# Kernel optimization log

Measured on AMD Instinct MI355X. Metric: run time of the kernel, lower is better.

Reference implementation:

```python
import jax, jax.numpy as jnp
import numpy as np

DIM = 128
BATCH = 1024


def _init_linear(key, fan_in, fan_out):
    kw, kb = jax.random.split(key)
    bound = 1.0 / np.sqrt(fan_in)
    W = jax.random.uniform(kw, (fan_in, fan_out), jnp.float32, -bound, bound)
    b = jax.random.uniform(kb, (fan_out,), jnp.float32, -bound, bound)
    return W, b


def setup_inputs() -> dict:
    key = jax.random.key(0)
    kx, ky, k1, k2, k3, k4 = jax.random.split(key, 6)
    x = jax.random.normal(kx, (BATCH, DIM), jnp.float32)
    y = jax.random.normal(ky, (BATCH, DIM), jnp.float32)
    W1, b1 = _init_linear(k1, 2 * DIM, 128)
    W2, b2 = _init_linear(k2, 128, 64)
    W3, b3 = _init_linear(k3, 64, 8)
    W4, b4 = _init_linear(k4, 8, 1)
    return {"x": x, "y": y, "W1": W1, "b1": b1, "W2": W2, "b2": b2,
            "W3": W3, "b3": b3, "W4": W4, "b4": b4}


def reference(x, y, W1, b1, W2, b2, W3, b3, W4, b4):
    # Original: pairs[i, j] = concat(x[j], y[i]); scores -> [B, B]; return transpose,
    # i.e. out[a, b] = f(concat(x[a], y[b])).
    # Split first linear algebraically: concat(x, y) @ W1 = x @ W1[:d] + y @ W1[d:].
    d = x.shape[1]
    xa = x @ W1[:d]          # [B, 128]
    yb = y @ W1[d:]          # [B, 128]
    h = jax.nn.relu(xa[:, None, :] + yb[None, :, :] + b1)  # [B, B, 128]
    h = jax.nn.relu(h @ W2 + b2)                            # [B, B, 64]
    h = jax.nn.relu(h @ W3 + b3)                            # [B, B, 8]
    out = (h @ W4 + b4)[..., 0]                             # [B, B]
    return out
```

## Files before the change

### kernel.cpp

```cpp
#include <hip/hip_runtime.h>
#include <hip/hip_bf16.h>

typedef float f32x4 __attribute__((ext_vector_type(4)));
typedef float f32x16 __attribute__((ext_vector_type(16)));
typedef short s16x8 __attribute__((ext_vector_type(8)));
typedef unsigned int u32x4 __attribute__((ext_vector_type(4)));

__device__ __forceinline__ short f2bf(float v) {
    __hip_bfloat16 h = __float2bfloat16(v);
    return __builtin_bit_cast(short, h);
}
__device__ __forceinline__ unsigned cvtpk(float lo, float hi) {
    unsigned r;
    asm("v_cvt_pk_bf16_f32 %0, %1, %2" : "=v"(r) : "v"(lo), "v"(hi));
    return r;
}
__device__ __forceinline__ void swap32(unsigned &x, unsigned &y) {
    asm("v_permlane32_swap_b32 %0, %1" : "+v"(x), "+v"(y));
}

__global__ __launch_bounds__(128) void precompute_kernel(
    const float* __restrict__ x, const float* __restrict__ y,
    const float* __restrict__ W1, const float* __restrict__ b1,
    float* __restrict__ xa, float* __restrict__ yb)
{
    __shared__ float rows[8][128];
    const int bid = blockIdx.x;
    const int k = threadIdx.x;
    const bool is_x = bid < 128;
    const int r0 = (is_x ? bid : bid - 128) * 8;
    const float* src = (is_x ? x : y) + (size_t)r0 * 128;
    const float* w = is_x ? W1 : (W1 + 128 * 128);
#pragma unroll
    for (int r = 0; r < 8; ++r) rows[r][k] = src[r * 128 + k];
    __syncthreads();
    float acc[8];
    const float bias = is_x ? b1[k] : 0.0f;
#pragma unroll
    for (int r = 0; r < 8; ++r) acc[r] = bias;
    for (int d = 0; d < 128; ++d) {
        float wv = w[d * 128 + k];
#pragma unroll
        for (int r = 0; r < 8; ++r) acc[r] = fmaf(rows[r][d], wv, acc[r]);
    }
    float* dst = (is_x ? xa : yb) + (size_t)r0 * 128 + k;
#pragma unroll
    for (int r = 0; r < 8; ++r) dst[r * 128] = acc[r];
}

__global__ __launch_bounds__(256, 2) void fused_kernel(
    const float* __restrict__ xa, const float* __restrict__ yb,
    const float* __restrict__ W2, const float* __restrict__ b2,
    const float* __restrict__ W3, const float* __restrict__ b3,
    const float* __restrict__ W4, const float* __restrict__ b4,
    float* __restrict__ out)
{
    __shared__ float xa_lds[16 * 128];
    __shared__ __align__(16) short w3_lds[4 * 64 * 8];

    const int tid = threadIdx.x;
    const int bid = blockIdx.x;
    const int a_chunk = bid >> 3;
    const int bq = bid & 7;
    const int wave = tid >> 6;
    const int lane = tid & 63;
    const int half = lane >> 5;
    const int m = lane & 31;
    const int bg = bq * 4 + wave;

    {
        const f32x4* xsrc = (const f32x4*)(xa + (size_t)a_chunk * 16 * 128);
        f32x4* dst = (f32x4*)xa_lds;
        dst[tid] = xsrc[tid];
        dst[tid + 256] = xsrc[tid + 256];
    }
    {
        int l = tid & 63, s = tid >> 6;
        int row = l & 31;
        int krow = s * 16 + (l >> 5) * 8;
        u32x4 q;
#pragma unroll
        for (int jj = 0; jj < 4; ++jj) {
            float lo = (row < 8) ? W3[(krow + 2 * jj) * 8 + row] : 0.f;
            float hi = (row < 8) ? W3[(krow + 2 * jj + 1) * 8 + row] : 0.f;
            q[jj] = cvtpk(lo, hi);
        }
        *(u32x4*)&w3_lds[tid * 8] = q;
    }

    f32x4 yv0[8], yv1[8];
    {
        const float* yrow = yb + (size_t)(bg * 32 + m) * 128 + half * 8;
#pragma unroll
        for (int s = 0; s < 8; ++s) {
            yv0[s] = *(const f32x4*)&yrow[s * 16];
            yv1[s] = *(const f32x4*)&yrow[s * 16 + 4];
        }
    }

    s16x8 W2a[2][8];
#pragma unroll
    for (int mt = 0; mt < 2; ++mt)
#pragma unroll
        for (int s = 0; s < 8; ++s)
#pragma unroll
            for (int j = 0; j < 8; ++j)
                W2a[mt][s][j] = f2bf(W2[(s * 16 + half * 8 + j) * 64 + mt * 32 + m]);

    f32x16 b2v0, b2v1;
#pragma unroll
    for (int r = 0; r < 16; ++r) {
        int f = (r & 3) + 8 * (r >> 2) + 4 * half;
        b2v0[r] = b2[f];
        b2v1[r] = b2[f + 32];
    }
    const f32x16 fz = {};
    float b3v[4], w4v[4];
#pragma unroll
    for (int j = 0; j < 4; ++j) {
        b3v[j] = b3[j + 4 * half];
        w4v[j] = W4[j + 4 * half];
    }
    const float b4s = b4[0];

    __syncthreads();

    const short* w3p = &w3_lds[lane * 8];
    float* outp = out + (size_t)(a_chunk * 16) * 1024 + bg * 32 + m;

    for (int ai = 0; ai < 16; ++ai) {
        const float* xr = &xa_lds[ai * 128 + half * 8];

        s16x8 bfr[8];
#pragma unroll
        for (int s = 0; s < 8; ++s) {
            f32x4 x0 = *(const f32x4*)&xr[s * 16];
            f32x4 x1 = *(const f32x4*)&xr[s * 16 + 4];
            f32x4 h0 = x0 + yv0[s];
            f32x4 h1 = x1 + yv1[s];
            u32x4 q;
            q.x = cvtpk(fmaxf(h0.x, 0.f), fmaxf(h0.y, 0.f));
            q.y = cvtpk(fmaxf(h0.z, 0.f), fmaxf(h0.w, 0.f));
            q.z = cvtpk(fmaxf(h1.x, 0.f), fmaxf(h1.y, 0.f));
            q.w = cvtpk(fmaxf(h1.z, 0.f), fmaxf(h1.w, 0.f));
            bfr[s] = __builtin_bit_cast(s16x8, q);
        }
        __builtin_amdgcn_sched_barrier(0);

        __builtin_amdgcn_s_setprio(1);
        f32x16 c20 = __builtin_amdgcn_mfma_f32_32x32x16_bf16(W2a[0][0], bfr[0], b2v0, 0, 0, 0);
        f32x16 c21 = __builtin_amdgcn_mfma_f32_32x32x16_bf16(W2a[1][0], bfr[0], b2v1, 0, 0, 0);
#pragma unroll
        for (int s = 1; s < 8; ++s) {
            c20 = __builtin_amdgcn_mfma_f32_32x32x16_bf16(W2a[0][s], bfr[s], c20, 0, 0, 0);
            c21 = __builtin_amdgcn_mfma_f32_32x32x16_bf16(W2a[1][s], bfr[s], c21, 0, 0, 0);
        }
        __builtin_amdgcn_s_setprio(0);

        unsigned P[8], Q[8];
#pragma unroll
        for (int i = 0; i < 8; ++i) {
            P[i] = cvtpk(fmaxf(c20[2 * i], 0.f), fmaxf(c20[2 * i + 1], 0.f));
            Q[i] = cvtpk(fmaxf(c21[2 * i], 0.f), fmaxf(c21[2 * i + 1], 0.f));
        }
        s16x8 bf3[4];
        {
            unsigned w0 = P[0], w2 = P[2]; swap32(w0, w2);
            unsigned w1 = P[1], w3 = P[3]; swap32(w1, w3);
            u32x4 t; t.x = w0; t.y = w1; t.z = w2; t.w = w3;
            bf3[0] = __builtin_bit_cast(s16x8, t);
            unsigned v0 = P[4], v2 = P[6]; swap32(v0, v2);
            unsigned v1 = P[5], v3 = P[7]; swap32(v1, v3);
            u32x4 u; u.x = v0; u.y = v1; u.z = v2; u.w = v3;
            bf3[1] = __builtin_bit_cast(s16x8, u);
            unsigned a0 = Q[0], a2 = Q[2]; swap32(a0, a2);
            unsigned a1 = Q[1], a3 = Q[3]; swap32(a1, a3);
            u32x4 t2; t2.x = a0; t2.y = a1; t2.z = a2; t2.w = a3;
            bf3[2] = __builtin_bit_cast(s16x8, t2);
            unsigned e0 = Q[4], e2 = Q[6]; swap32(e0, e2);
            unsigned e1 = Q[5], e3 = Q[7]; swap32(e1, e3);
            u32x4 u2; u2.x = e0; u2.y = e1; u2.z = e2; u2.w = e3;
            bf3[3] = __builtin_bit_cast(s16x8, u2);
        }

        __builtin_amdgcn_s_setprio(1);
        f32x16 c3 = __builtin_amdgcn_mfma_f32_32x32x16_bf16(
            *(const s16x8*)(w3p + 0 * 512), bf3[0], fz, 0, 0, 0);
#pragma unroll
        for (int s = 1; s < 4; ++s)
            c3 = __builtin_amdgcn_mfma_f32_32x32x16_bf16(
                *(const s16x8*)(w3p + s * 512), bf3[s], c3, 0, 0, 0);
        __builtin_amdgcn_s_setprio(0);

        float p = 0.f;
#pragma unroll
        for (int j = 0; j < 4; ++j)
            p = fmaf(fmaxf(c3[j] + b3v[j], 0.f), w4v[j], p);
        unsigned pu = __builtin_bit_cast(unsigned, p);
        unsigned pv = pu;
        asm("" : "+v"(pv));
        swap32(pu, pv);
        float r = __builtin_bit_cast(float, pu) + __builtin_bit_cast(float, pv) + b4s;
        if (half == 0)
            outp[(size_t)ai * 1024] = r;
    }
}

extern "C" void kernel_launch(void* const* d_in, const int* in_sizes, int n_in,
                              void* d_out, int out_size, void* d_ws, size_t ws_size,
                              hipStream_t stream) {
    const float* x  = (const float*)d_in[0];
    const float* y  = (const float*)d_in[1];
    const float* W1 = (const float*)d_in[2];
    const float* b1 = (const float*)d_in[3];
    const float* W2 = (const float*)d_in[4];
    const float* b2 = (const float*)d_in[5];
    const float* W3 = (const float*)d_in[6];
    const float* b3 = (const float*)d_in[7];
    const float* W4 = (const float*)d_in[8];
    const float* b4 = (const float*)d_in[9];
    float* out = (float*)d_out;

    float* xa = (float*)d_ws;
    float* yb = xa + 1024 * 128;

    precompute_kernel<<<dim3(256), dim3(128), 0, stream>>>(x, y, W1, b1, xa, yb);
    fused_kernel<<<dim3(512), dim3(256), 0, stream>>>(xa, yb, W2, b2, W3, b3, W4, b4, out);
}
```

Before: 44.17 us.

## Interleave two independent rows per iteration and stage biases in LDS

The fused loop now processes two x rows (ai and ai+8) per iteration, interleaving their MFMA chains so the two independent accumulator streams can hide MFMA dependency latency. The b2/b3 bias vectors move from per-thread registers into LDS and are reloaded each iteration to cut register pressure. The W3 fragments are hoisted, and the setprio and sched_barrier hints are dropped. The cost is more live registers for the doubled bfr and accumulators, which may threaten the occupancy of 2 waves implied by the launch bounds.

```diff
diff --git a/kernel.cpp b/kernel.cpp
--- a/kernel.cpp
+++ b/kernel.cpp
@@ -57,6 +57,8 @@
 {
     __shared__ float xa_lds[16 * 128];
     __shared__ __align__(16) short w3_lds[4 * 64 * 8];
+    __shared__ __align__(64) float b2_lds[64];
+    __shared__ __align__(64) float b3_lds[32];
 
     const int tid = threadIdx.x;
     const int bid = blockIdx.x;
@@ -87,6 +89,10 @@
         }
         *(u32x4*)&w3_lds[tid * 8] = q;
     }
+    if (tid < 64)
+        b2_lds[tid] = b2[(tid & 3) + 8 * ((tid >> 2) & 3) + 4 * ((tid >> 4) & 1) + 32 * (tid >> 5)];
+    if (tid < 32)
+        b3_lds[tid] = ((tid & 15) < 4) ? b3[(tid & 3) + 4 * (tid >> 4)] : 0.f;
 
     f32x4 yv0[8], yv1[8];
     {
@@ -107,20 +113,9 @@
             for (int j = 0; j < 8; ++j)
                 W2a[mt][s][j] = f2bf(W2[(s * 16 + half * 8 + j) * 64 + mt * 32 + m]);
 
-    f32x16 b2v0, b2v1;
-#pragma unroll
-    for (int r = 0; r < 16; ++r) {
-        int f = (r & 3) + 8 * (r >> 2) + 4 * half;
-        b2v0[r] = b2[f];
-        b2v1[r] = b2[f + 32];
-    }
-    const f32x16 fz = {};
-    float b3v[4], w4v[4];
-#pragma unroll
-    for (int j = 0; j < 4; ++j) {
-        b3v[j] = b3[j + 4 * half];
-        w4v[j] = W4[j + 4 * half];
-    }
+    float w4v[4];
+#pragma unroll
+    for (int j = 0; j < 4; ++j) w4v[j] = W4[j + 4 * half];
     const float b4s = b4[0];
 
     __syncthreads();
@@ -128,81 +123,128 @@
     const short* w3p = &w3_lds[lane * 8];
     float* outp = out + (size_t)(a_chunk * 16) * 1024 + bg * 32 + m;
 
-    for (int ai = 0; ai < 16; ++ai) {
-        const float* xr = &xa_lds[ai * 128 + half * 8];
-
-        s16x8 bfr[8];
-#pragma unroll
-        for (int s = 0; s < 8; ++s) {
-            f32x4 x0 = *(const f32x4*)&xr[s * 16];
-            f32x4 x1 = *(const f32x4*)&xr[s * 16 + 4];
-            f32x4 h0 = x0 + yv0[s];
-            f32x4 h1 = x1 + yv1[s];
-            u32x4 q;
-            q.x = cvtpk(fmaxf(h0.x, 0.f), fmaxf(h0.y, 0.f));
-            q.y = cvtpk(fmaxf(h0.z, 0.f), fmaxf(h0.w, 0.f));
-            q.z = cvtpk(fmaxf(h1.x, 0.f), fmaxf(h1.y, 0.f));
-            q.w = cvtpk(fmaxf(h1.z, 0.f), fmaxf(h1.w, 0.f));
-            bfr[s] = __builtin_bit_cast(s16x8, q);
-        }
-        __builtin_amdgcn_sched_barrier(0);
-
-        __builtin_amdgcn_s_setprio(1);
-        f32x16 c20 = __builtin_amdgcn_mfma_f32_32x32x16_bf16(W2a[0][0], bfr[0], b2v0, 0, 0, 0);
-        f32x16 c21 = __builtin_amdgcn_mfma_f32_32x32x16_bf16(W2a[1][0], bfr[0], b2v1, 0, 0, 0);
+    for (int ai = 0; ai < 8; ++ai) {
+        s16x8 bfrA[8], bfrB[8];
+        {
+            const float* xrA = &xa_lds[ai * 128 + half * 8];
+            const float* xrB = &xa_lds[(ai + 8) * 128 + half * 8];
+#pragma unroll
+            for (int s = 0; s < 8; ++s) {
+                f32x4 a0 = *(const f32x4*)&xrA[s * 16] + yv0[s];
+                f32x4 a1 = *(const f32x4*)&xrA[s * 16 + 4] + yv1[s];
+                u32x4 qa;
+                qa.x = cvtpk(fmaxf(a0.x, 0.f), fmaxf(a0.y, 0.f));
+                qa.y = cvtpk(fmaxf(a0.z, 0.f), fmaxf(a0.w, 0.f));
+                qa.z = cvtpk(fmaxf(a1.x, 0.f), fmaxf(a1.y, 0.f));
+                qa.w = cvtpk(fmaxf(a1.z, 0.f), fmaxf(a1.w, 0.f));
+                bfrA[s] = __builtin_bit_cast(s16x8, qa);
+                f32x4 b0 = *(const f32x4*)&xrB[s * 16] + yv0[s];
+                f32x4 b1 = *(const f32x4*)&xrB[s * 16 + 4] + yv1[s];
+                u32x4 qb;
+                qb.x = cvtpk(fmaxf(b0.x, 0.f), fmaxf(b0.y, 0.f));
+                qb.y = cvtpk(fmaxf(b0.z, 0.f), fmaxf(b0.w, 0.f));
+                qb.z = cvtpk(fmaxf(b1.x, 0.f), fmaxf(b1.y, 0.f));
+                qb.w = cvtpk(fmaxf(b1.z, 0.f), fmaxf(b1.w, 0.f));
+                bfrB[s] = __builtin_bit_cast(s16x8, qb);
+            }
+        }
+
+        const f32x16 cb0 = *(const f32x16*)&b2_lds[half * 16];
+        const f32x16 cb1 = *(const f32x16*)&b2_lds[32 + half * 16];
+        f32x16 c20A = __builtin_amdgcn_mfma_f32_32x32x16_bf16(W2a[0][0], bfrA[0], cb0, 0, 0, 0);
+        f32x16 c21A = __builtin_amdgcn_mfma_f32_32x32x16_bf16(W2a[1][0], bfrA[0], cb1, 0, 0, 0);
+        f32x16 c20B = __builtin_amdgcn_mfma_f32_32x32x16_bf16(W2a[0][0], bfrB[0], cb0, 0, 0, 0);
+        f32x16 c21B = __builtin_amdgcn_mfma_f32_32x32x16_bf16(W2a[1][0], bfrB[0], cb1, 0, 0, 0);
 #pragma unroll
         for (int s = 1; s < 8; ++s) {
-            c20 = __builtin_amdgcn_mfma_f32_32x32x16_bf16(W2a[0][s], bfr[s], c20, 0, 0, 0);
-            c21 = __builtin_amdgcn_mfma_f32_32x32x16_bf16(W2a[1][s], bfr[s], c21, 0, 0, 0);
-        }
-        __builtin_amdgcn_s_setprio(0);
-
-        unsigned P[8], Q[8];
-#pragma unroll
-        for (int i = 0; i < 8; ++i) {
-            P[i] = cvtpk(fmaxf(c20[2 * i], 0.f), fmaxf(c20[2 * i + 1], 0.f));
-            Q[i] = cvtpk(fmaxf(c21[2 * i], 0.f), fmaxf(c21[2 * i + 1], 0.f));
-        }
-        s16x8 bf3[4];
+            c20A = __builtin_amdgcn_mfma_f32_32x32x16_bf16(W2a[0][s], bfrA[s], c20A, 0, 0, 0);
+            c21A = __builtin_amdgcn_mfma_f32_32x32x16_bf16(W2a[1][s], bfrA[s], c21A, 0, 0, 0);
+            c20B = __builtin_amdgcn_mfma_f32_32x32x16_bf16(W2a[0][s], bfrB[s], c20B, 0, 0, 0);
+            c21B = __builtin_amdgcn_mfma_f32_32x32x16_bf16(W2a[1][s], bfrB[s], c21B, 0, 0, 0);
+        }
+
+        s16x8 bf3A[4], bf3B[4];
         {
+            unsigned P[8], Q[8];
+#pragma unroll
+            for (int i = 0; i < 8; ++i) {
+                P[i] = cvtpk(fmaxf(c20A[2 * i], 0.f), fmaxf(c20A[2 * i + 1], 0.f));
+                Q[i] = cvtpk(fmaxf(c21A[2 * i], 0.f), fmaxf(c21A[2 * i + 1], 0.f));
+            }
             unsigned w0 = P[0], w2 = P[2]; swap32(w0, w2);
             unsigned w1 = P[1], w3 = P[3]; swap32(w1, w3);
             u32x4 t; t.x = w0; t.y = w1; t.z = w2; t.w = w3;
-            bf3[0] = __builtin_bit_cast(s16x8, t);
+            bf3A[0] = __builtin_bit_cast(s16x8, t);
             unsigned v0 = P[4], v2 = P[6]; swap32(v0, v2);
             unsigned v1 = P[5], v3 = P[7]; swap32(v1, v3);
             u32x4 u; u.x = v0; u.y = v1; u.z = v2; u.w = v3;
-            bf3[1] = __builtin_bit_cast(s16x8, u);
+            bf3A[1] = __builtin_bit_cast(s16x8, u);
             unsigned a0 = Q[0], a2 = Q[2]; swap32(a0, a2);
             unsigned a1 = Q[1], a3 = Q[3]; swap32(a1, a3);
             u32x4 t2; t2.x = a0; t2.y = a1; t2.z = a2; t2.w = a3;
-            bf3[2] = __builtin_bit_cast(s16x8, t2);
+            bf3A[2] = __builtin_bit_cast(s16x8, t2);
             unsigned e0 = Q[4], e2 = Q[6]; swap32(e0, e2);
             unsigned e1 = Q[5], e3 = Q[7]; swap32(e1, e3);
             u32x4 u2; u2.x = e0; u2.y = e1; u2.z = e2; u2.w = e3;
-            bf3[3] = __builtin_bit_cast(s16x8, u2);
-        }
-
-        __builtin_amdgcn_s_setprio(1);
-        f32x16 c3 = __builtin_amdgcn_mfma_f32_32x32x16_bf16(
-            *(const s16x8*)(w3p + 0 * 512), bf3[0], fz, 0, 0, 0);
-#pragma unroll
-        for (int s = 1; s < 4; ++s)
-            c3 = __builtin_amdgcn_mfma_f32_32x32x16_bf16(
-                *(const s16x8*)(w3p + s * 512), bf3[s], c3, 0, 0, 0);
-        __builtin_amdgcn_s_setprio(0);
-
-        float p = 0.f;
-#pragma unroll
-        for (int j = 0; j < 4; ++j)
-            p = fmaf(fmaxf(c3[j] + b3v[j], 0.f), w4v[j], p);
-        unsigned pu = __builtin_bit_cast(unsigned, p);
-        unsigned pv = pu;
-        asm("" : "+v"(pv));
-        swap32(pu, pv);
-        float r = __builtin_bit_cast(float, pu) + __builtin_bit_cast(float, pv) + b4s;
-        if (half == 0)
-            outp[(size_t)ai * 1024] = r;
+            bf3A[3] = __builtin_bit_cast(s16x8, u2);
+        }
+        {
+            unsigned P[8], Q[8];
+#pragma unroll
+            for (int i = 0; i < 8; ++i) {
+                P[i] = cvtpk(fmaxf(c20B[2 * i], 0.f), fmaxf(c20B[2 * i + 1], 0.f));
+                Q[i] = cvtpk(fmaxf(c21B[2 * i], 0.f), fmaxf(c21B[2 * i + 1], 0.f));
+            }
+            unsigned w0 = P[0], w2 = P[2]; swap32(w0, w2);
+            unsigned w1 = P[1], w3 = P[3]; swap32(w1, w3);
+            u32x4 t; t.x = w0; t.y = w1; t.z = w2; t.w = w3;
+            bf3B[0] = __builtin_bit_cast(s16x8, t);
+            unsigned v0 = P[4], v2 = P[6]; swap32(v0, v2);
+            unsigned v1 = P[5], v3 = P[7]; swap32(v1, v3);
+            u32x4 u; u.x = v0; u.y = v1; u.z = v2; u.w = v3;
+            bf3B[1] = __builtin_bit_cast(s16x8, u);
+            unsigned a0 = Q[0], a2 = Q[2]; swap32(a0, a2);
+            unsigned a1 = Q[1], a3 = Q[3]; swap32(a1, a3);
+            u32x4 t2; t2.x = a0; t2.y = a1; t2.z = a2; t2.w = a3;
+            bf3B[2] = __builtin_bit_cast(s16x8, t2);
+            unsigned e0 = Q[4], e2 = Q[6]; swap32(e0, e2);
+            unsigned e1 = Q[5], e3 = Q[7]; swap32(e1, e3);
+            u32x4 u2; u2.x = e0; u2.y = e1; u2.z = e2; u2.w = e3;
+            bf3B[3] = __builtin_bit_cast(s16x8, u2);
+        }
+
+        const f32x16 c3i = *(const f32x16*)&b3_lds[half * 16];
+        const s16x8 w3f0 = *(const s16x8*)(w3p + 0 * 512);
+        const s16x8 w3f1 = *(const s16x8*)(w3p + 1 * 512);
+        const s16x8 w3f2 = *(const s16x8*)(w3p + 2 * 512);
+        const s16x8 w3f3 = *(const s16x8*)(w3p + 3 * 512);
+        f32x16 c3A = __builtin_amdgcn_mfma_f32_32x32x16_bf16(w3f0, bf3A[0], c3i, 0, 0, 0);
+        f32x16 c3B = __builtin_amdgcn_mfma_f32_32x32x16_bf16(w3f0, bf3B[0], c3i, 0, 0, 0);
+        c3A = __builtin_amdgcn_mfma_f32_32x32x16_bf16(w3f1, bf3A[1], c3A, 0, 0, 0);
+        c3B = __builtin_amdgcn_mfma_f32_32x32x16_bf16(w3f1, bf3B[1], c3B, 0, 0, 0);
+        c3A = __builtin_amdgcn_mfma_f32_32x32x16_bf16(w3f2, bf3A[2], c3A, 0, 0, 0);
+        c3B = __builtin_amdgcn_mfma_f32_32x32x16_bf16(w3f2, bf3B[2], c3B, 0, 0, 0);
+        c3A = __builtin_amdgcn_mfma_f32_32x32x16_bf16(w3f3, bf3A[3], c3A, 0, 0, 0);
+        c3B = __builtin_amdgcn_mfma_f32_32x32x16_bf16(w3f3, bf3B[3], c3B, 0, 0, 0);
+
+        float pA = fmaxf(c3A[0], 0.f) * w4v[0] + fmaxf(c3A[1], 0.f) * w4v[1]
+                 + fmaxf(c3A[2], 0.f) * w4v[2] + fmaxf(c3A[3], 0.f) * w4v[3];
+        float pB = fmaxf(c3B[0], 0.f) * w4v[0] + fmaxf(c3B[1], 0.f) * w4v[1]
+                 + fmaxf(c3B[2], 0.f) * w4v[2] + fmaxf(c3B[3], 0.f) * w4v[3];
+        unsigned puA = __builtin_bit_cast(unsigned, pA);
+        unsigned pvA = puA;
+        asm("" : "+v"(pvA));
+        swap32(puA, pvA);
+        unsigned puB = __builtin_bit_cast(unsigned, pB);
+        unsigned pvB = puB;
+        asm("" : "+v"(pvB));
+        swap32(puB, pvB);
+        float rA = __builtin_bit_cast(float, puA) + __builtin_bit_cast(float, pvA) + b4s;
+        float rB = __builtin_bit_cast(float, puB) + __builtin_bit_cast(float, pvB) + b4s;
+        if (half == 0) {
+            outp[(size_t)ai * 1024] = rA;
+            outp[(size_t)(ai + 8) * 1024] = rB;
+        }
     }
 }
 
```

After: 40.25 us. 1.1x faster.
